# Performance work log

Measured on AMD Instinct MI355X. Metric: run time of the kernel, lower is better.

The kernel has to match this reference:

```python
import jax, jax.numpy as jnp
import numpy as np

N_NODES = 100000
N_EDGES = 3200000
NFEAT, NHID, NOUT = 256, 128, 64


def spmm(edge_row, edge_col, edge_val, dense):
    # out[r] = sum_{e: row[e]==r} val[e] * dense[col[e]]
    gathered = dense[edge_col] * edge_val[:, None]  # [E, F]
    return jax.ops.segment_sum(gathered, edge_row, num_segments=N_NODES)


def setup_inputs() -> dict:
    key = jax.random.key(0)
    ks = jax.random.split(key, 8)
    stdv1 = 1.0 / np.sqrt(NHID)
    stdv2 = 1.0 / np.sqrt(NOUT)
    return {
        "x": jax.random.normal(ks[0], (N_NODES, NFEAT), dtype=jnp.float32),
        "edge_row": jax.random.randint(ks[1], (N_EDGES,), 0, N_NODES, dtype=jnp.int32),
        "edge_col": jax.random.randint(ks[2], (N_EDGES,), 0, N_NODES, dtype=jnp.int32),
        "edge_val": jax.random.uniform(ks[3], (N_EDGES,), dtype=jnp.float32),
        "W1": jax.random.uniform(ks[4], (NFEAT, NHID), jnp.float32, -stdv1, stdv1),
        "b1": jax.random.uniform(ks[5], (NHID,), jnp.float32, -stdv1, stdv1),
        "W2": jax.random.uniform(ks[6], (NHID, NOUT), jnp.float32, -stdv2, stdv2),
        "b2": jax.random.uniform(ks[7], (NOUT,), jnp.float32, -stdv2, stdv2),
    }


def reference(x, edge_row, edge_col, edge_val, W1, b1, W2, b2):
    # layer 1: dense projection, SpMM aggregate, bias, ReLU
    support = x @ W1                                   # [N, NHID]
    h = spmm(edge_row, edge_col, edge_val, support) + b1
    h = jax.nn.relu(h)
    # dropout skipped (eval mode: training=False)
    # layer 2
    support2 = h @ W2                                  # [N, NOUT]
    out = spmm(edge_row, edge_col, edge_val, support2) + b2
    return out
```

## Files before the change

### kernel.cpp

```cpp
#include <hip/hip_runtime.h>
#include <hip/hip_bf16.h>

#define N_NODES 100000
#define N_EDGES 3200000
#define NFEAT 256
#define NHID 128
#define NOUT 64

#define BSHIFT 8
#define BROWS 256
#define NBUCK 391
#define EPB 4096
#define NBLK1 ((N_EDGES + EPB - 1) / EPB)
#define GB1 782

typedef __attribute__((ext_vector_type(8))) short short8;
typedef __attribute__((ext_vector_type(8))) unsigned short ushort8_t;
typedef __attribute__((ext_vector_type(4))) float f32x4;

__device__ __forceinline__ unsigned short f2bf(float f) {
    union { float f; unsigned int u; } v; v.f = f;
    unsigned int r = v.u + 0x7fffu + ((v.u >> 16) & 1u);
    return (unsigned short)(r >> 16);
}
__device__ __forceinline__ float bflo(unsigned int u) { return __uint_as_float(u << 16); }
__device__ __forceinline__ float bfhi(unsigned int u) { return __uint_as_float(u & 0xffff0000u); }


__global__ __launch_bounds__(256) void bcount_cvtw(const int* __restrict__ erow,
                                                   int* __restrict__ Mt,
                                                   const float* __restrict__ W1,
                                                   const float* __restrict__ W2,
                                                   unsigned short* __restrict__ W1b,
                                                   unsigned short* __restrict__ W2b) {
    __shared__ int h[NBUCK];
    if (blockIdx.x >= NBLK1) {
        const int i = (blockIdx.x - NBLK1) * 256 + threadIdx.x;
        if (i < NFEAT * NHID) W1b[i] = f2bf(W1[i]);
        if (i < NHID * NOUT)  W2b[i] = f2bf(W2[i]);
        return;
    }
    for (int i = threadIdx.x; i < NBUCK; i += 256) h[i] = 0;
    __syncthreads();
    const int base = blockIdx.x * EPB;
    const int n = min(EPB, N_EDGES - base);
    for (int i = threadIdx.x; i < n; i += 256)
        atomicAdd(&h[erow[base + i] >> BSHIFT], 1);
    __syncthreads();
    for (int b = threadIdx.x; b < NBUCK; b += 256)
        Mt[(size_t)b * NBLK1 + blockIdx.x] = h[b];
}


__global__ __launch_bounds__(256) void colscan_kernel(int* __restrict__ Mt,
                                                      int* __restrict__ btot) {
    const int wv = threadIdx.x >> 6, lane = threadIdx.x & 63;
    const int b = blockIdx.x * 4 + wv;
    if (b >= NBUCK) return;
    int* row = Mt + (size_t)b * NBLK1;
    int carry = 0;
    for (int t = 0; t < NBLK1; t += 64) {
        int i = t + lane;
        int v = (i < NBLK1) ? row[i] : 0;
        int x = v;
        #pragma unroll
        for (int off = 1; off < 64; off <<= 1) {
            int tt = __shfl_up(x, off);
            if (lane >= off) x += tt;
        }
        if (i < NBLK1) row[i] = carry + x - v;
        carry += __shfl(x, 63);
    }
    if (lane == 0) btot[b] = carry;
}


__global__ __launch_bounds__(1024) void bscan_kernel(const int* __restrict__ btot,
                                                     int* __restrict__ bbase) {
    __shared__ int wsum[16];
    const int tid = threadIdx.x;
    const int lane = tid & 63;
    int v = (tid < NBUCK) ? btot[tid] : 0;
    int x = v;
    #pragma unroll
    for (int off = 1; off < 64; off <<= 1) {
        int t = __shfl_up(x, off);
        if (lane >= off) x += t;
    }
    if (lane == 63) wsum[tid >> 6] = x;
    __syncthreads();
    if (tid < 16) {
        int s = wsum[tid];
        #pragma unroll
        for (int off = 1; off < 16; off <<= 1) {
            int t = __shfl_up(s, off);
            if (tid >= off) s += t;
        }
        wsum[tid] = s;
    }
    __syncthreads();
    if (tid >= 64) x += wsum[(tid >> 6) - 1];
    if (tid < NBUCK) bbase[tid] = x - v;
    if (tid == NBUCK - 1) bbase[NBUCK] = x;
}


__global__ __launch_bounds__(256) void binsort_kernel(const int* __restrict__ erow,
                                                      const int* __restrict__ ecol,
                                                      const float* __restrict__ eval,
                                                      const int* __restrict__ Mt,
                                                      const int* __restrict__ btot,
                                                      const int* __restrict__ bbase,
                                                      int2* __restrict__ tmp) {
    __shared__ int2 sc[EPB];
    __shared__ unsigned short sb[EPB];
    __shared__ int hist[NBUCK];
    __shared__ int delta[NBUCK];
    __shared__ int scan_t[4];

    const int blk = blockIdx.x;
    const int tid = threadIdx.x;
    const int base = blk * EPB;
    const int n = min(EPB, N_EDGES - base);

    int v0 = 0, v1 = 0, v2 = 0, v3 = 0;
    int m0 = 0, m1 = 0, m2 = 0, m3 = 0;
    {
        const int i0 = tid * 4;
        #define LOADCNT(k, vk, mk) { \
            int idx = i0 + k; \
            if (idx < NBUCK) { \
                mk = Mt[(size_t)idx * NBLK1 + blk]; \
                int nx = (blk + 1 < NBLK1) ? Mt[(size_t)idx * NBLK1 + blk + 1] : btot[idx]; \
                vk = nx - mk; \
            } }
        LOADCNT(0, v0, m0) LOADCNT(1, v1, m1) LOADCNT(2, v2, m2) LOADCNT(3, v3, m3)
        #undef LOADCNT
    }
    int s4 = v0 + v1 + v2 + v3;
    int xi = s4;
    const int lane = tid & 63;
    #pragma unroll
    for (int off = 1; off < 64; off <<= 1) {
        int t = __shfl_up(xi, off);
        if (lane >= off) xi += t;
    }
    if (lane == 63) scan_t[tid >> 6] = xi;
    __syncthreads();
    if (tid == 0) {
        int run = 0;
        #pragma unroll
        for (int w = 0; w < 4; ++w) { int t = scan_t[w]; scan_t[w] = run; run += t; }
    }
    __syncthreads();
    {
        int e0 = scan_t[tid >> 6] + xi - s4;
        int i0 = tid * 4;
        int ex[4] = {e0, e0 + v0, e0 + v0 + v1, e0 + v0 + v1 + v2};
        int mm[4] = {m0, m1, m2, m3};
        #pragma unroll
        for (int k = 0; k < 4; ++k) {
            int idx = i0 + k;
            if (idx < NBUCK) {
                hist[idx] = ex[k];
                delta[idx] = bbase[idx] + mm[k] - ex[k];
            }
        }
    }
    __syncthreads();

    for (int i = tid; i < n; i += 256) {
        int r = erow[base + i];
        int b = r >> BSHIFT;
        int rl = r & (BROWS - 1);
        int pos = atomicAdd(&hist[b], 1);
        sc[pos] = make_int2((rl << 17) | ecol[base + i], __float_as_int(eval[base + i]));
        sb[pos] = (unsigned short)b;
    }
    __syncthreads();

    for (int i = tid; i < n; i += 256) {
        int b = sb[i];
        tmp[delta[b] + i] = sc[i];
    }
}


__device__ __forceinline__ void gemm1_role(int bid, char* sm,
                                           const float* __restrict__ X,
                                           const unsigned short* __restrict__ Wb,
                                           unsigned short* __restrict__ Y) {
    unsigned short* bt = (unsigned short*)sm;
    const int tid = threadIdx.x;
    const int lane = tid & 63;
    const int w = tid >> 6;
    const int rb = bid * 128 + w * 32;
    const int lr = lane & 15;
    const int kg = lane >> 4;
    const int M = N_NODES;

    f32x4 acc[2][8];
    #pragma unroll
    for (int a = 0; a < 2; ++a)
        #pragma unroll
        for (int nf = 0; nf < 8; ++nf)
            #pragma unroll
            for (int i = 0; i < 4; ++i) acc[a][nf][i] = 0.f;

    for (int ph = 0; ph < 2; ++ph) {
        if (ph) __syncthreads();
        {
            const int nn = tid & 127;
            const int kb = tid >> 7;
            #pragma unroll
            for (int kk0 = 0; kk0 < 64; kk0 += 8) {
                const int kk = kb * 64 + kk0;
                unsigned short p[8];
                #pragma unroll
                for (int i = 0; i < 8; ++i)
                    p[i] = Wb[(size_t)(ph * 128 + kk + i) * NHID + nn];
                unsigned int byte = (unsigned int)nn * 256 + (unsigned int)kk * 2;
                byte ^= (unsigned int)(nn & 7) << 4;
                *(ushort8_t*)((char*)bt + byte) = *(const ushort8_t*)p;
            }
        }
        __syncthreads();

        #pragma unroll
        for (int ks = 0; ks < 4; ++ks) {
            const int k0 = ph * 128 + ks * 32 + kg * 8;
            short8 a0, a1;
            #pragma unroll
            for (int af = 0; af < 2; ++af) {
                const int row = rb + af * 16 + lr;
                short8 r;
                if (row < M) {
                    const float* p = X + (size_t)row * NFEAT + k0;
                    float4 u0 = *(const float4*)p;
                    float4 u1 = *(const float4*)(p + 4);
                    unsigned short q[8] = {f2bf(u0.x), f2bf(u0.y), f2bf(u0.z), f2bf(u0.w),
                                           f2bf(u1.x), f2bf(u1.y), f2bf(u1.z), f2bf(u1.w)};
                    r = *(const short8*)q;
                } else {
                    #pragma unroll
                    for (int i = 0; i < 8; ++i) r[i] = 0;
                }
                if (af == 0) a0 = r; else a1 = r;
            }
            #pragma unroll
            for (int nf = 0; nf < 8; ++nf) {
                const int nn = nf * 16 + lr;
                unsigned int byte = (unsigned int)nn * 256 + (unsigned int)(ks * 32 + kg * 8) * 2;
                byte ^= (unsigned int)(nn & 7) << 4;
                short8 bfr = *(const short8*)((const char*)bt + byte);
                acc[0][nf] = __builtin_amdgcn_mfma_f32_16x16x32_bf16(a0, bfr, acc[0][nf], 0, 0, 0);
                acc[1][nf] = __builtin_amdgcn_mfma_f32_16x16x32_bf16(a1, bfr, acc[1][nf], 0, 0, 0);
            }
        }
    }

    #pragma unroll
    for (int af = 0; af < 2; ++af)
        #pragma unroll
        for (int nf = 0; nf < 8; ++nf)
            #pragma unroll
            for (int i = 0; i < 4; ++i) {
                const int r = rb + af * 16 + kg * 4 + i;
                if (r < M) Y[(size_t)r * NHID + nf * 16 + lr] = f2bf(acc[af][nf][i]);
            }
}

__device__ __forceinline__ void rowsort_role(int b, char* sm,
                                             const int* __restrict__ bbase,
                                             const int2* __restrict__ tmp,
                                             int2* __restrict__ ec2,
                                             int* __restrict__ rowptr) {
    int* h  = (int*)sm;
    int* hx = (int*)(sm + 1024);
    int* wq = (int*)(sm + 2048);

    const int s = bbase[b], e = bbase[b + 1];
    const int n = e - s;
    const int tid = threadIdx.x;
    const int lane = tid & 63;

    h[tid] = 0;
    __syncthreads();
    for (int i = tid; i < n; i += 256)
        atomicAdd(&h[((unsigned)tmp[s + i].x) >> 17], 1);
    __syncthreads();

    int v = h[tid];
    int x = v;
    #pragma unroll
    for (int off = 1; off < 64; off <<= 1) {
        int t = __shfl_up(x, off);
        if (lane >= off) x += t;
    }
    if (lane == 63) wq[tid >> 6] = x;
    __syncthreads();
    if (tid == 0) {
        int run = 0;
        #pragma unroll
        for (int w = 0; w < 4; ++w) { int t = wq[w]; wq[w] = run; run += t; }
    }
    __syncthreads();
    x += wq[tid >> 6];
    {
        const int grow = b * BROWS + tid;
        if (grow < N_NODES) rowptr[grow + 1] = s + x;
        if (b == 0 && tid == 0) rowptr[0] = 0;
        hx[tid] = s + (x - v);
    }
    __syncthreads();

    for (int i = tid; i < n; i += 256) {
        int2 d = tmp[s + i];
        unsigned int rl = ((unsigned)d.x) >> 17;
        int pos = atomicAdd(&hx[rl], 1);
        ec2[pos] = make_int2(d.x & 0x1FFFF, d.y);
    }
}

__global__ __launch_bounds__(256) void rowsort_g1(const int* __restrict__ bbase,
                                                  const int2* __restrict__ tmp,
                                                  int2* __restrict__ ec2,
                                                  int* __restrict__ rowptr,
                                                  const float* __restrict__ X,
                                                  const unsigned short* __restrict__ W1b,
                                                  unsigned short* __restrict__ Y) {
    extern __shared__ char sm[];
    if (blockIdx.x < GB1) gemm1_role(blockIdx.x, sm, X, W1b, Y);
    else                  rowsort_role(blockIdx.x - GB1, sm, bbase, tmp, ec2, rowptr);
}


template<int N, int K>
__global__ __launch_bounds__(256) void gemm_mfma(const unsigned short* __restrict__ X,
                                                 const unsigned short* __restrict__ Wb,
                                                 unsigned short* __restrict__ Y, int M) {
    __shared__ unsigned short bt[N * K];
    const int tid = threadIdx.x;

    {
        const int n = tid & (N - 1);
        const int kb = tid / N;
        const int kspan = K / (256 / N);
        for (int k0 = kb * kspan; k0 < (kb + 1) * kspan; k0 += 8) {
            unsigned short p[8];
            #pragma unroll
            for (int i = 0; i < 8; ++i) p[i] = Wb[(size_t)(k0 + i) * N + n];
            unsigned int byte = (unsigned int)n * (K * 2) + (unsigned int)k0 * 2;
            byte ^= (unsigned int)(n & 7) << 4;
            *(ushort8_t*)((char*)bt + byte) = *(const ushort8_t*)p;
        }
    }
    __syncthreads();

    const int lane = tid & 63;
    const int w = tid >> 6;
    const int rb = blockIdx.x * 128 + w * 32;
    const int lr = lane & 15;
    const int kg = lane >> 4;
    constexpr int NF = N / 16;
    constexpr int KS = K / 32;

    f32x4 acc[2][NF];
    #pragma unroll
    for (int a = 0; a < 2; ++a)
        #pragma unroll
        for (int nf = 0; nf < NF; ++nf)
            #pragma unroll
            for (int i = 0; i < 4; ++i) acc[a][nf][i] = 0.f;

    auto loadA = [&](int af, int ks) -> short8 {
        const int row = rb + af * 16 + lr;
        const int k0 = ks * 32 + kg * 8;
        short8 r;
        if (row < M) {
            r = *(const short8*)(X + (size_t)row * K + k0);
        } else {
            #pragma unroll
            for (int i = 0; i < 8; ++i) r[i] = 0;
        }
        return r;
    };
    auto loadB = [&](int nf, int ks) -> short8 {
        const int n = nf * 16 + lr;
        unsigned int byte = (unsigned int)n * (K * 2) + (unsigned int)(ks * 32 + kg * 8) * 2;
        byte ^= (unsigned int)(n & 7) << 4;
        return *(const short8*)((const char*)bt + byte);
    };

    #pragma unroll
    for (int ks = 0; ks < KS; ++ks) {
        short8 a0 = loadA(0, ks), a1 = loadA(1, ks);
        #pragma unroll
        for (int nf = 0; nf < NF; ++nf) {
            short8 bfr = loadB(nf, ks);
            acc[0][nf] = __builtin_amdgcn_mfma_f32_16x16x32_bf16(a0, bfr, acc[0][nf], 0, 0, 0);
            acc[1][nf] = __builtin_amdgcn_mfma_f32_16x16x32_bf16(a1, bfr, acc[1][nf], 0, 0, 0);
        }
    }

    #pragma unroll
    for (int af = 0; af < 2; ++af)
        #pragma unroll
        for (int nf = 0; nf < NF; ++nf)
            #pragma unroll
            for (int i = 0; i < 4; ++i) {
                const int r = rb + af * 16 + kg * 4 + i;
                if (r < M) Y[(size_t)r * N + nf * 16 + lr] = f2bf(acc[af][nf][i]);
            }
}


__global__ __launch_bounds__(256) void spmm1_kernel(const int* __restrict__ rp,
                                                    const int2* __restrict__ ec,
                                                    const unsigned int* __restrict__ d32,
                                                    const float* __restrict__ bias,
                                                    unsigned short* __restrict__ out) {
    const int lane = threadIdx.x & 63;
    const int row = blockIdx.x * 4 + (threadIdx.x >> 6);
    if (row >= N_NODES) return;
    const int s = __builtin_amdgcn_readfirstlane(rp[row]);
    const int e = __builtin_amdgcn_readfirstlane(rp[row + 1]);
    float a0 = 0.f, a1 = 0.f, b0 = 0.f, b1 = 0.f;
    float c0a = 0.f, c1a = 0.f, d0a = 0.f, d1a = 0.f;
    int j = s;
    for (; j + 16 <= e; j += 16) {
        int2 q0 = ec[j],      q1 = ec[j + 1],  q2 = ec[j + 2],  q3 = ec[j + 3];
        int2 q4 = ec[j + 4],  q5 = ec[j + 5],  q6 = ec[j + 6],  q7 = ec[j + 7];
        int2 q8 = ec[j + 8],  q9 = ec[j + 9],  qa = ec[j + 10], qb = ec[j + 11];
        int2 qc = ec[j + 12], qd = ec[j + 13], qe = ec[j + 14], qf = ec[j + 15];
        unsigned int u0 = d32[(size_t)q0.x * 64 + lane];
        unsigned int u1 = d32[(size_t)q1.x * 64 + lane];
        unsigned int u2 = d32[(size_t)q2.x * 64 + lane];
        unsigned int u3 = d32[(size_t)q3.x * 64 + lane];
        unsigned int u4 = d32[(size_t)q4.x * 64 + lane];
        unsigned int u5 = d32[(size_t)q5.x * 64 + lane];
        unsigned int u6 = d32[(size_t)q6.x * 64 + lane];
        unsigned int u7 = d32[(size_t)q7.x * 64 + lane];
        unsigned int u8 = d32[(size_t)q8.x * 64 + lane];
        unsigned int u9 = d32[(size_t)q9.x * 64 + lane];
        unsigned int ua = d32[(size_t)qa.x * 64 + lane];
        unsigned int ub = d32[(size_t)qb.x * 64 + lane];
        unsigned int uc = d32[(size_t)qc.x * 64 + lane];
        unsigned int ud = d32[(size_t)qd.x * 64 + lane];
        unsigned int ue = d32[(size_t)qe.x * 64 + lane];
        unsigned int uf = d32[(size_t)qf.x * 64 + lane];
        float v0 = __int_as_float(q0.y), v1 = __int_as_float(q1.y);
        float v2 = __int_as_float(q2.y), v3 = __int_as_float(q3.y);
        float v4 = __int_as_float(q4.y), v5 = __int_as_float(q5.y);
        float v6 = __int_as_float(q6.y), v7 = __int_as_float(q7.y);
        float v8 = __int_as_float(q8.y), v9 = __int_as_float(q9.y);
        float va = __int_as_float(qa.y), vb = __int_as_float(qb.y);
        float vc = __int_as_float(qc.y), vd = __int_as_float(qd.y);
        float ve = __int_as_float(qe.y), vf = __int_as_float(qf.y);
        a0 += v0 * bflo(u0); a1 += v0 * bfhi(u0);
        b0 += v1 * bflo(u1); b1 += v1 * bfhi(u1);
        c0a += v2 * bflo(u2); c1a += v2 * bfhi(u2);
        d0a += v3 * bflo(u3); d1a += v3 * bfhi(u3);
        a0 += v4 * bflo(u4); a1 += v4 * bfhi(u4);
        b0 += v5 * bflo(u5); b1 += v5 * bfhi(u5);
        c0a += v6 * bflo(u6); c1a += v6 * bfhi(u6);
        d0a += v7 * bflo(u7); d1a += v7 * bfhi(u7);
        a0 += v8 * bflo(u8); a1 += v8 * bfhi(u8);
        b0 += v9 * bflo(u9); b1 += v9 * bfhi(u9);
        c0a += va * bflo(ua); c1a += va * bfhi(ua);
        d0a += vb * bflo(ub); d1a += vb * bfhi(ub);
        a0 += vc * bflo(uc); a1 += vc * bfhi(uc);
        b0 += vd * bflo(ud); b1 += vd * bfhi(ud);
        c0a += ve * bflo(ue); c1a += ve * bfhi(ue);
        d0a += vf * bflo(uf); d1a += vf * bfhi(uf);
    }
    for (; j + 8 <= e; j += 8) {
        int2 q0 = ec[j],     q1 = ec[j + 1], q2 = ec[j + 2], q3 = ec[j + 3];
        int2 q4 = ec[j + 4], q5 = ec[j + 5], q6 = ec[j + 6], q7 = ec[j + 7];
        unsigned int u0 = d32[(size_t)q0.x * 64 + lane];
        unsigned int u1 = d32[(size_t)q1.x * 64 + lane];
        unsigned int u2 = d32[(size_t)q2.x * 64 + lane];
        unsigned int u3 = d32[(size_t)q3.x * 64 + lane];
        unsigned int u4 = d32[(size_t)q4.x * 64 + lane];
        unsigned int u5 = d32[(size_t)q5.x * 64 + lane];
        unsigned int u6 = d32[(size_t)q6.x * 64 + lane];
        unsigned int u7 = d32[(size_t)q7.x * 64 + lane];
        float v0 = __int_as_float(q0.y), v1 = __int_as_float(q1.y);
        float v2 = __int_as_float(q2.y), v3 = __int_as_float(q3.y);
        float v4 = __int_as_float(q4.y), v5 = __int_as_float(q5.y);
        float v6 = __int_as_float(q6.y), v7 = __int_as_float(q7.y);
        a0 += v0 * bflo(u0); a1 += v0 * bfhi(u0);
        b0 += v1 * bflo(u1); b1 += v1 * bfhi(u1);
        c0a += v2 * bflo(u2); c1a += v2 * bfhi(u2);
        d0a += v3 * bflo(u3); d1a += v3 * bfhi(u3);
        a0 += v4 * bflo(u4); a1 += v4 * bfhi(u4);
        b0 += v5 * bflo(u5); b1 += v5 * bfhi(u5);
        c0a += v6 * bflo(u6); c1a += v6 * bfhi(u6);
        d0a += v7 * bflo(u7); d1a += v7 * bfhi(u7);
    }
    for (; j < e; ++j) {
        int2 c = ec[j];
        float v = __int_as_float(c.y);
        unsigned int u = d32[(size_t)c.x * 64 + lane];
        a0 += v * bflo(u);
        a1 += v * bfhi(u);
    }
    a0 += b0 + c0a + d0a; a1 += b1 + c1a + d1a;
    float2 bp = *(const float2*)(bias + 2 * lane);
    float r0 = fmaxf(a0 + bp.x, 0.f);
    float r1 = fmaxf(a1 + bp.y, 0.f);
    unsigned int pack = (unsigned int)f2bf(r0) | ((unsigned int)f2bf(r1) << 16);
    *(unsigned int*)(out + (size_t)row * 128 + 2 * lane) = pack;
}


__global__ __launch_bounds__(256) void spmm2_kernel(const int* __restrict__ rp,
                                                    const int2* __restrict__ ec,
                                                    const unsigned int* __restrict__ d32,
                                                    const float* __restrict__ bias,
                                                    float* __restrict__ out) {
    const int lane = threadIdx.x & 63;
    const int row = blockIdx.x * 4 + (threadIdx.x >> 6);
    if (row >= N_NODES) return;
    const int s = __builtin_amdgcn_readfirstlane(rp[row]);
    const int e = __builtin_amdgcn_readfirstlane(rp[row + 1]);
    const int eh = lane >> 5, cl = lane & 31;
    float a0 = 0.f, a1 = 0.f, b0 = 0.f, b1 = 0.f;
    float c0a = 0.f, c1a = 0.f, d0a = 0.f, d1a = 0.f;
    int j = s;
    for (; j + 16 <= e; j += 16) {
        int2 q0 = ec[j + eh],      q1 = ec[j + 2 + eh];
        int2 q2 = ec[j + 4 + eh],  q3 = ec[j + 6 + eh];
        int2 q4 = ec[j + 8 + eh],  q5 = ec[j + 10 + eh];
        int2 q6 = ec[j + 12 + eh], q7 = ec[j + 14 + eh];
        unsigned int u0 = d32[(size_t)q0.x * 32 + cl];
        unsigned int u1 = d32[(size_t)q1.x * 32 + cl];
        unsigned int u2 = d32[(size_t)q2.x * 32 + cl];
        unsigned int u3 = d32[(size_t)q3.x * 32 + cl];
        unsigned int u4 = d32[(size_t)q4.x * 32 + cl];
        unsigned int u5 = d32[(size_t)q5.x * 32 + cl];
        unsigned int u6 = d32[(size_t)q6.x * 32 + cl];
        unsigned int u7 = d32[(size_t)q7.x * 32 + cl];
        float v0 = __int_as_float(q0.y), v1 = __int_as_float(q1.y);
        float v2 = __int_as_float(q2.y), v3 = __int_as_float(q3.y);
        float v4 = __int_as_float(q4.y), v5 = __int_as_float(q5.y);
        float v6 = __int_as_float(q6.y), v7 = __int_as_float(q7.y);
        a0 += v0 * bflo(u0); a1 += v0 * bfhi(u0);
        b0 += v1 * bflo(u1); b1 += v1 * bfhi(u1);
        c0a += v2 * bflo(u2); c1a += v2 * bfhi(u2);
        d0a += v3 * bflo(u3); d1a += v3 * bfhi(u3);
        a0 += v4 * bflo(u4); a1 += v4 * bfhi(u4);
        b0 += v5 * bflo(u5); b1 += v5 * bfhi(u5);
        c0a += v6 * bflo(u6); c1a += v6 * bfhi(u6);
        d0a += v7 * bflo(u7); d1a += v7 * bfhi(u7);
    }
    for (; j + 8 <= e; j += 8) {
        int2 q0 = ec[j + eh],     q1 = ec[j + 2 + eh];
        int2 q2 = ec[j + 4 + eh], q3 = ec[j + 6 + eh];
        unsigned int u0 = d32[(size_t)q0.x * 32 + cl];
        unsigned int u1 = d32[(size_t)q1.x * 32 + cl];
        unsigned int u2 = d32[(size_t)q2.x * 32 + cl];
        unsigned int u3 = d32[(size_t)q3.x * 32 + cl];
        float v0 = __int_as_float(q0.y), v1 = __int_as_float(q1.y);
        float v2 = __int_as_float(q2.y), v3 = __int_as_float(q3.y);
        a0 += v0 * bflo(u0); a1 += v0 * bfhi(u0);
        b0 += v1 * bflo(u1); b1 += v1 * bfhi(u1);
        c0a += v2 * bflo(u2); c1a += v2 * bfhi(u2);
        d0a += v3 * bflo(u3); d1a += v3 * bfhi(u3);
    }
    for (; j < e; j += 2) {
        const int j2 = j + eh;
        if (j2 < e) {
            int2 cv = ec[j2];
            float v = __int_as_float(cv.y);
            unsigned int u = d32[(size_t)cv.x * 32 + cl];
            a0 += v * bflo(u);
            a1 += v * bfhi(u);
        }
    }
    a0 += b0 + c0a + d0a; a1 += b1 + c1a + d1a;
    a0 += __shfl_xor(a0, 32);
    a1 += __shfl_xor(a1, 32);
    if (eh == 0) {
        float2 bp = *(const float2*)(bias + 2 * cl);
        *(float2*)(out + (size_t)row * 64 + 2 * cl) = make_float2(a0 + bp.x, a1 + bp.y);
    }
}


extern "C" void kernel_launch(void* const* d_in, const int* in_sizes, int n_in,
                              void* d_out, int out_size, void* d_ws, size_t ws_size,
                              hipStream_t stream) {
    const float* x    = (const float*)d_in[0];
    const int*   erow = (const int*)d_in[1];
    const int*   ecol = (const int*)d_in[2];
    const float* evalv = (const float*)d_in[3];
    const float* W1   = (const float*)d_in[4];
    const float* b1   = (const float*)d_in[5];
    const float* W2   = (const float*)d_in[6];
    const float* b2   = (const float*)d_in[7];
    float* out = (float*)d_out;

    char* wsp = (char*)d_ws;
    size_t off = 0;
    auto alloc = [&](size_t bytes) -> void* {
        void* p = wsp + off;
        off = (off + bytes + 255) & ~(size_t)255;
        return p;
    };
    unsigned short* support = (unsigned short*)alloc((size_t)N_NODES * NHID * 2);
    unsigned short* hbuf    = (unsigned short*)alloc((size_t)N_NODES * NHID * 2);
    int2*  tmp     = (int2*)alloc((size_t)N_EDGES * 8);
    int2*  ec2     = (int2*)alloc((size_t)N_EDGES * 8);
    int*   Mt      = (int*)alloc((size_t)NBUCK * NBLK1 * 4);
    int*   btot    = (int*)alloc((size_t)NBUCK * 4);
    int*   bbase   = (int*)alloc((size_t)(NBUCK + 1) * 4);
    int*   rowptr  = (int*)alloc((size_t)(N_NODES + 1) * 4);
    unsigned short* W1b = (unsigned short*)alloc((size_t)NFEAT * NHID * 2);
    unsigned short* W2b = (unsigned short*)alloc((size_t)NHID * NOUT * 2);

    bcount_cvtw<<<NBLK1 + 128, 256, 0, stream>>>(erow, Mt, W1, W2, W1b, W2b);
    colscan_kernel<<<(NBUCK + 3) / 4, 256, 0, stream>>>(Mt, btot);
    bscan_kernel<<<1, 1024, 0, stream>>>(btot, bbase);
    binsort_kernel<<<NBLK1, 256, 0, stream>>>(erow, ecol, evalv, Mt, btot, bbase, tmp);
    rowsort_g1<<<GB1 + NBUCK, 256, 32768, stream>>>(bbase, tmp, ec2, rowptr,
                                                    x, W1b, support);

    spmm1_kernel<<<(N_NODES + 3) / 4, 256, 0, stream>>>(rowptr, ec2, (const unsigned int*)support, b1, hbuf);
    gemm_mfma<NOUT, NHID><<<(N_NODES + 127) / 128, 256, 0, stream>>>(hbuf, W2b, support, N_NODES);
    spmm2_kernel<<<(N_NODES + 3) / 4, 256, 0, stream>>>(rowptr, ec2, (const unsigned int*)support, b2, out);
}
```

Measured before the change: 309.6 us.

## Fuse second-layer projection into SpMM1 epilogue and drop separate GEMM kernel

The h @ W2 projection now runs inside the first SpMM kernel. Each block stores its four ReLU'd hidden rows in shared memory, then computes the 64-wide output per row with scalar FMAs against a transposed bf16 W2. This removes the hbuf round trip and one kernel launch, and spmm2 now reads the smaller sup2 buffer. In exchange, the MFMA GEMM becomes per-thread scalar dot products with W2 rows re-read from cache, and a block-wide barrier is added to the SpMM kernel.

```diff
diff --git a/kernel.cpp b/kernel.cpp
--- a/kernel.cpp
+++ b/kernel.cpp
@@ -25,6 +25,7 @@
 }
 __device__ __forceinline__ float bflo(unsigned int u) { return __uint_as_float(u << 16); }
 __device__ __forceinline__ float bfhi(unsigned int u) { return __uint_as_float(u & 0xffff0000u); }
+__device__ __forceinline__ float bfup(unsigned short u) { return __uint_as_float(((unsigned)u) << 16); }
 
 
 __global__ __launch_bounds__(256) void bcount_cvtw(const int* __restrict__ erow,
@@ -32,12 +33,15 @@
                                                    const float* __restrict__ W1,
                                                    const float* __restrict__ W2,
                                                    unsigned short* __restrict__ W1b,
-                                                   unsigned short* __restrict__ W2b) {
+                                                   unsigned short* __restrict__ W2bT) {
     __shared__ int h[NBUCK];
     if (blockIdx.x >= NBLK1) {
         const int i = (blockIdx.x - NBLK1) * 256 + threadIdx.x;
         if (i < NFEAT * NHID) W1b[i] = f2bf(W1[i]);
-        if (i < NHID * NOUT)  W2b[i] = f2bf(W2[i]);
+        if (i < NHID * NOUT) {
+            const int k = i >> 6, n = i & 63;
+            W2bT[n * NHID + k] = f2bf(W2[i]);
+        }
         return;
     }
     for (int i = threadIdx.x; i < NBUCK; i += 256) h[i] = 0;
@@ -335,94 +339,16 @@
 }
 
 
-template<int N, int K>
-__global__ __launch_bounds__(256) void gemm_mfma(const unsigned short* __restrict__ X,
-                                                 const unsigned short* __restrict__ Wb,
-                                                 unsigned short* __restrict__ Y, int M) {
-    __shared__ unsigned short bt[N * K];
-    const int tid = threadIdx.x;
-
-    {
-        const int n = tid & (N - 1);
-        const int kb = tid / N;
-        const int kspan = K / (256 / N);
-        for (int k0 = kb * kspan; k0 < (kb + 1) * kspan; k0 += 8) {
-            unsigned short p[8];
-            #pragma unroll
-            for (int i = 0; i < 8; ++i) p[i] = Wb[(size_t)(k0 + i) * N + n];
-            unsigned int byte = (unsigned int)n * (K * 2) + (unsigned int)k0 * 2;
-            byte ^= (unsigned int)(n & 7) << 4;
-            *(ushort8_t*)((char*)bt + byte) = *(const ushort8_t*)p;
-        }
-    }
-    __syncthreads();
-
-    const int lane = tid & 63;
-    const int w = tid >> 6;
-    const int rb = blockIdx.x * 128 + w * 32;
-    const int lr = lane & 15;
-    const int kg = lane >> 4;
-    constexpr int NF = N / 16;
-    constexpr int KS = K / 32;
-
-    f32x4 acc[2][NF];
-    #pragma unroll
-    for (int a = 0; a < 2; ++a)
-        #pragma unroll
-        for (int nf = 0; nf < NF; ++nf)
-            #pragma unroll
-            for (int i = 0; i < 4; ++i) acc[a][nf][i] = 0.f;
-
-    auto loadA = [&](int af, int ks) -> short8 {
-        const int row = rb + af * 16 + lr;
-        const int k0 = ks * 32 + kg * 8;
-        short8 r;
-        if (row < M) {
-            r = *(const short8*)(X + (size_t)row * K + k0);
-        } else {
-            #pragma unroll
-            for (int i = 0; i < 8; ++i) r[i] = 0;
-        }
-        return r;
-    };
-    auto loadB = [&](int nf, int ks) -> short8 {
-        const int n = nf * 16 + lr;
-        unsigned int byte = (unsigned int)n * (K * 2) + (unsigned int)(ks * 32 + kg * 8) * 2;
-        byte ^= (unsigned int)(n & 7) << 4;
-        return *(const short8*)((const char*)bt + byte);
-    };
-
-    #pragma unroll
-    for (int ks = 0; ks < KS; ++ks) {
-        short8 a0 = loadA(0, ks), a1 = loadA(1, ks);
-        #pragma unroll
-        for (int nf = 0; nf < NF; ++nf) {
-            short8 bfr = loadB(nf, ks);
-            acc[0][nf] = __builtin_amdgcn_mfma_f32_16x16x32_bf16(a0, bfr, acc[0][nf], 0, 0, 0);
-            acc[1][nf] = __builtin_amdgcn_mfma_f32_16x16x32_bf16(a1, bfr, acc[1][nf], 0, 0, 0);
-        }
-    }
-
-    #pragma unroll
-    for (int af = 0; af < 2; ++af)
-        #pragma unroll
-        for (int nf = 0; nf < NF; ++nf)
-            #pragma unroll
-            for (int i = 0; i < 4; ++i) {
-                const int r = rb + af * 16 + kg * 4 + i;
-                if (r < M) Y[(size_t)r * N + nf * 16 + lr] = f2bf(acc[af][nf][i]);
-            }
-}
-
-
 __global__ __launch_bounds__(256) void spmm1_kernel(const int* __restrict__ rp,
                                                     const int2* __restrict__ ec,
                                                     const unsigned int* __restrict__ d32,
                                                     const float* __restrict__ bias,
-                                                    unsigned short* __restrict__ out) {
+                                                    const unsigned short* __restrict__ W2bT,
+                                                    unsigned short* __restrict__ out2) {
+    __shared__ float hrow[4][128];
     const int lane = threadIdx.x & 63;
-    const int row = blockIdx.x * 4 + (threadIdx.x >> 6);
-    if (row >= N_NODES) return;
+    const int wv = threadIdx.x >> 6;
+    const int row = blockIdx.x * 4 + wv;
     const int s = __builtin_amdgcn_readfirstlane(rp[row]);
     const int e = __builtin_amdgcn_readfirstlane(rp[row + 1]);
     float a0 = 0.f, a1 = 0.f, b0 = 0.f, b1 = 0.f;
@@ -509,8 +435,26 @@
     float2 bp = *(const float2*)(bias + 2 * lane);
     float r0 = fmaxf(a0 + bp.x, 0.f);
     float r1 = fmaxf(a1 + bp.y, 0.f);
-    unsigned int pack = (unsigned int)f2bf(r0) | ((unsigned int)f2bf(r1) << 16);
-    *(unsigned int*)(out + (size_t)row * 128 + 2 * lane) = pack;
+    *(float2*)&hrow[wv][2 * lane] = make_float2(r0, r1);
+    __syncthreads();
+
+    {
+        const int rr = threadIdx.x >> 6;
+        const int n  = threadIdx.x & 63;
+        const unsigned short* wt = W2bT + n * NHID;
+        float acc2 = 0.f;
+        #pragma unroll
+        for (int k = 0; k < NHID; k += 8) {
+            ushort8_t w8 = *(const ushort8_t*)(wt + k);
+            float4 h0 = *(const float4*)&hrow[rr][k];
+            float4 h1 = *(const float4*)&hrow[rr][k + 4];
+            acc2 += h0.x * bfup(w8[0]) + h0.y * bfup(w8[1])
+                  + h0.z * bfup(w8[2]) + h0.w * bfup(w8[3])
+                  + h1.x * bfup(w8[4]) + h1.y * bfup(w8[5])
+                  + h1.z * bfup(w8[6]) + h1.w * bfup(w8[7]);
+        }
+        out2[(size_t)(blockIdx.x * 4 + rr) * NOUT + n] = f2bf(acc2);
+    }
 }
 
 
@@ -609,24 +553,25 @@
         return p;
     };
     unsigned short* support = (unsigned short*)alloc((size_t)N_NODES * NHID * 2);
-    unsigned short* hbuf    = (unsigned short*)alloc((size_t)N_NODES * NHID * 2);
+    unsigned short* sup2    = (unsigned short*)alloc((size_t)N_NODES * NOUT * 2);
     int2*  tmp     = (int2*)alloc((size_t)N_EDGES * 8);
     int2*  ec2     = (int2*)alloc((size_t)N_EDGES * 8);
     int*   Mt      = (int*)alloc((size_t)NBUCK * NBLK1 * 4);
     int*   btot    = (int*)alloc((size_t)NBUCK * 4);
     int*   bbase   = (int*)alloc((size_t)(NBUCK + 1) * 4);
     int*   rowptr  = (int*)alloc((size_t)(N_NODES + 1) * 4);
-    unsigned short* W1b = (unsigned short*)alloc((size_t)NFEAT * NHID * 2);
-    unsigned short* W2b = (unsigned short*)alloc((size_t)NHID * NOUT * 2);
-
-    bcount_cvtw<<<NBLK1 + 128, 256, 0, stream>>>(erow, Mt, W1, W2, W1b, W2b);
+    unsigned short* W1b  = (unsigned short*)alloc((size_t)NFEAT * NHID * 2);
+    unsigned short* W2bT = (unsigned short*)alloc((size_t)NHID * NOUT * 2);
+
+    bcount_cvtw<<<NBLK1 + 128, 256, 0, stream>>>(erow, Mt, W1, W2, W1b, W2bT);
     colscan_kernel<<<(NBUCK + 3) / 4, 256, 0, stream>>>(Mt, btot);
     bscan_kernel<<<1, 1024, 0, stream>>>(btot, bbase);
     binsort_kernel<<<NBLK1, 256, 0, stream>>>(erow, ecol, evalv, Mt, btot, bbase, tmp);
     rowsort_g1<<<GB1 + NBUCK, 256, 32768, stream>>>(bbase, tmp, ec2, rowptr,
                                                     x, W1b, support);
 
-    spmm1_kernel<<<(N_NODES + 3) / 4, 256, 0, stream>>>(rowptr, ec2, (const unsigned int*)support, b1, hbuf);
-    gemm_mfma<NOUT, NHID><<<(N_NODES + 127) / 128, 256, 0, stream>>>(hbuf, W2b, support, N_NODES);
-    spmm2_kernel<<<(N_NODES + 3) / 4, 256, 0, stream>>>(rowptr, ec2, (const unsigned int*)support, b2, out);
-}
+    spmm1_kernel<<<N_NODES / 4, 256, 0, stream>>>(rowptr, ec2, (const unsigned int*)support,
+                                                  b1, W2bT, sup2);
+    spmm2_kernel<<<N_NODES / 4, 256, 0, stream>>>(rowptr, ec2, (const unsigned int*)sup2,
+                                                  b2, out);
+}
```

Result: slower. 418.1 us (+35.1%).
